# Optimization experiments

Measured on AMD Instinct MI355X. Metric: run time of the kernel, lower is better.

Reference implementation:

```python
import jax, jax.numpy as jnp
import numpy as np

N_NODES = 100000
N_EDGES = 200000
N_GRAPHS = 4096
NODE_DIM = 64
HID = 256
N_GAT = 4
NEG_SLOPE = 0.2
EPS = 1e-9


def setup_inputs() -> dict:
    key = jax.random.key(0)
    ks = jax.random.split(key, 16)
    node_feats = jax.random.normal(ks[0], (N_NODES, NODE_DIM), dtype=jnp.float32)
    src = jax.random.randint(ks[1], (N_EDGES,), 0, N_NODES)
    dst = jax.random.randint(ks[2], (N_EDGES,), 0, N_NODES)
    graph_ids = jnp.sort(jax.random.randint(ks[3], (N_NODES,), 0, N_GRAPHS))
    s = 1.0 / np.sqrt(HID)
    w_embed = jax.random.normal(ks[4], (NODE_DIM, HID), dtype=jnp.float32) / np.sqrt(NODE_DIM)
    b_embed = jnp.zeros((HID,), dtype=jnp.float32)
    gat_W = jax.random.normal(ks[5], (N_GAT, HID, HID), dtype=jnp.float32) * s
    gat_al = jax.random.normal(ks[6], (N_GAT, HID), dtype=jnp.float32) * s
    gat_ar = jax.random.normal(ks[7], (N_GAT, HID), dtype=jnp.float32) * s
    w1 = jax.random.normal(ks[8], (HID, HID // 2), dtype=jnp.float32) * s
    b1 = jnp.zeros((HID // 2,), dtype=jnp.float32)
    w2 = jax.random.normal(ks[9], (HID // 2, HID // 4), dtype=jnp.float32) / np.sqrt(HID // 2)
    b2 = jnp.zeros((HID // 4,), dtype=jnp.float32)
    w3 = jax.random.normal(ks[10], (HID // 4, 1), dtype=jnp.float32) / np.sqrt(HID // 4)
    b3 = jnp.zeros((1,), dtype=jnp.float32)
    return dict(node_feats=node_feats, src=src, dst=dst, graph_ids=graph_ids,
                w_embed=w_embed, b_embed=b_embed, gat_W=gat_W, gat_al=gat_al,
                gat_ar=gat_ar, w1=w1, b1=b1, w2=w2, b2=b2, w3=w3, b3=b3)


def _gat_layer(h, W, al, ar, src, dst):
    z = h @ W                                   # [N, HID]
    el = z @ al                                 # [N] source attention term
    er = z @ ar                                 # [N] destination attention term
    e = jax.nn.leaky_relu(el[src] + er[dst], NEG_SLOPE)   # [E]
    # segment softmax over edges grouped by destination node
    emax = jax.ops.segment_max(e, dst, num_segments=N_NODES)
    emax = jnp.where(jnp.isfinite(emax), emax, 0.0)
    ex = jnp.exp(e - emax[dst])
    esum = jax.ops.segment_sum(ex, dst, num_segments=N_NODES)
    alpha = ex / (esum[dst] + EPS)              # [E]
    m = jax.ops.segment_sum(alpha[:, None] * z[src], dst, num_segments=N_NODES)
    return jax.nn.relu(m + h)                   # residual + ReLU


def reference(node_feats, src, dst, graph_ids, w_embed, b_embed,
              gat_W, gat_al, gat_ar, w1, b1, w2, b2, w3, b3):
    h = node_feats @ w_embed + b_embed          # node embedding
    for l in range(N_GAT):
        h = _gat_layer(h, gat_W[l], gat_al[l], gat_ar[l], src, dst)
    g = jax.ops.segment_sum(h, graph_ids, num_segments=N_GRAPHS)  # sum pooling [G, HID]
    g = jax.nn.relu(g @ w1 + b1)
    g = jax.nn.relu(g @ w2 + b2)
    return g @ w3 + b3                          # [G, 1]
```

## Files before the change

### kernel.cpp

```cpp
#include <hip/hip_runtime.h>
#include <hip/hip_bf16.h>

#define N_NODES 100000
#define N_EDGES 200000
#define N_GRAPHS 4096
#define NODE_DIM 64
#define HID 256
#define N_GAT 4
#define NEG_SLOPE 0.2f
#define EPS 1e-9f
#define NB 98

typedef const __attribute__((address_space(1))) void gv_t;
typedef __attribute__((address_space(3))) void lv_t;
typedef __attribute__((ext_vector_type(8))) short bf16x8;
typedef __attribute__((ext_vector_type(4))) float f32x4;

__device__ __forceinline__ float b2f(unsigned short u) {
    return __uint_as_float(((unsigned)u) << 16);
}
__device__ __forceinline__ unsigned short f2b(float f) {
    unsigned u = __float_as_uint(f);
    return (unsigned short)((u + 0x7fffu + ((u >> 16) & 1u)) >> 16);
}

__global__ void convert_f32_bf16(const float* __restrict__ src,
                                 unsigned short* __restrict__ dst, int n4) {
    int i = blockIdx.x * 256 + threadIdx.x;
    if (i >= n4) return;
    float4 v = ((const float4*)src)[i];
    ushort4 o;
    o.x = f2b(v.x); o.y = f2b(v.y); o.z = f2b(v.z); o.w = f2b(v.w);
    ((ushort4*)dst)[i] = o;
}

__global__ __launch_bounds__(256) void transpose_bf16(const float* __restrict__ W,
                                                      unsigned short* __restrict__ Wt,
                                                      int K) {
    __shared__ float tile[32][33];
    const int kb = blockIdx.x * 32, cb = blockIdx.y * 32;
    const int tr = threadIdx.x >> 5, tc = threadIdx.x & 31;
#pragma unroll
    for (int i = 0; i < 4; ++i)
        tile[tr + i * 8][tc] = W[(size_t)(kb + tr + i * 8) * HID + cb + tc];
    __syncthreads();
#pragma unroll
    for (int i = 0; i < 4; ++i)
        Wt[(size_t)(cb + tr + i * 8) * K + kb + tc] = f2b(tile[tc][tr + i * 8]);
}

template <int K, bool BIAS, bool DOTS>
__global__ __launch_bounds__(256) void gemm_mfma(const unsigned short* __restrict__ Xb,
                                                 const unsigned short* __restrict__ Wt,
                                                 const float* __restrict__ bias,
                                                 unsigned short* __restrict__ Yb,
                                                 const float* __restrict__ al,
                                                 const float* __restrict__ ar,
                                                 float* __restrict__ el,
                                                 float* __restrict__ er,
                                                 int M) {
    constexpr int KC = 64;
    constexpr int NT = K / KC;
    __shared__ unsigned short xs[2][128 * KC];
    __shared__ unsigned short wsx[2][128 * KC];
    const int t = threadIdx.x, wv = t >> 6, ln = t & 63;
    const int wr2 = wv >> 1, wc2 = wv & 1;
    const long row0 = (long)blockIdx.x * 128;
    const int  col0 = blockIdx.y * 128;

    auto stage = [&](int buf, int k0) {
#pragma unroll
        for (int i = 0; i < 4; ++i) {
            const int chunk = wv * 4 + i;
            const int row = chunk * 8 + (ln >> 3);
            const int gsrc = (ln & 7) ^ (row & 7);
            long gr = row0 + row; if (gr >= M) gr = M - 1;
            const unsigned short* gp = Xb + gr * K + k0 + gsrc * 8;
            __builtin_amdgcn_global_load_lds((gv_t*)gp, (lv_t*)(&xs[buf][chunk * 512 + ln * 8]), 16, 0, 0);
        }
#pragma unroll
        for (int i = 0; i < 4; ++i) {
            const int chunk = wv * 4 + i;
            const int row = chunk * 8 + (ln >> 3);
            const int gsrc = (ln & 7) ^ (row & 7);
            const unsigned short* gp = Wt + (size_t)(col0 + row) * K + k0 + gsrc * 8;
            __builtin_amdgcn_global_load_lds((gv_t*)gp, (lv_t*)(&wsx[buf][chunk * 512 + ln * 8]), 16, 0, 0);
        }
    };

    f32x4 acc[4][4];
#pragma unroll
    for (int m = 0; m < 4; ++m)
#pragma unroll
        for (int n = 0; n < 4; ++n) acc[m][n] = (f32x4){0.f, 0.f, 0.f, 0.f};

    stage(0, 0);
    __syncthreads();

#pragma unroll
    for (int tt = 0; tt < NT; ++tt) {
        const int cur = tt & 1;
        if (tt + 1 < NT) stage(cur ^ 1, (tt + 1) * KC);

#pragma unroll
        for (int kk = 0; kk < 2; ++kk) {
            bf16x8 a[4], b[4];
            const int g = kk * 4 + (ln >> 4);
#pragma unroll
            for (int m = 0; m < 4; ++m) {
                const int row = wr2 * 64 + m * 16 + (ln & 15);
                const int s = g ^ (row & 7);
                a[m] = *(const bf16x8*)&xs[cur][row * 64 + s * 8];
            }
#pragma unroll
            for (int n = 0; n < 4; ++n) {
                const int row = wc2 * 64 + n * 16 + (ln & 15);
                const int s = g ^ (row & 7);
                b[n] = *(const bf16x8*)&wsx[cur][row * 64 + s * 8];
            }
#pragma unroll
            for (int m = 0; m < 4; ++m)
#pragma unroll
                for (int n = 0; n < 4; ++n)
                    acc[m][n] = __builtin_amdgcn_mfma_f32_16x16x32_bf16(a[m], b[n], acc[m][n], 0, 0, 0);
        }
        __syncthreads();
    }

    float bj[4];
#pragma unroll
    for (int n = 0; n < 4; ++n)
        bj[n] = BIAS ? bias[col0 + wc2 * 64 + n * 16 + (ln & 15)] : 0.f;

#pragma unroll
    for (int m = 0; m < 4; ++m) {
        const long rbase = row0 + wr2 * 64 + m * 16 + 4 * (ln >> 4);
#pragma unroll
        for (int n = 0; n < 4; ++n) {
            const int col = col0 + wc2 * 64 + n * 16 + (ln & 15);
#pragma unroll
            for (int q = 0; q < 4; ++q) {
                const long r = rbase + q;
                if (r >= M) continue;
                Yb[r * HID + col] = f2b(acc[m][n][q] + bj[n]);
            }
        }
    }

    if (DOTS) {
        float alv[4], arv[4];
#pragma unroll
        for (int n = 0; n < 4; ++n) {
            const int col = col0 + wc2 * 64 + n * 16 + (ln & 15);
            alv[n] = al[col];
            arv[n] = ar[col];
        }
#pragma unroll
        for (int m = 0; m < 4; ++m) {
#pragma unroll
            for (int q = 0; q < 4; ++q) {
                float pl = 0.f, pr = 0.f;
#pragma unroll
                for (int n = 0; n < 4; ++n) {
                    pl = fmaf(acc[m][n][q], alv[n], pl);
                    pr = fmaf(acc[m][n][q], arv[n], pr);
                }
#pragma unroll
                for (int o = 1; o < 16; o <<= 1) {
                    pl += __shfl_xor(pl, o);
                    pr += __shfl_xor(pr, o);
                }
                if ((ln & 15) == 0) {
                    const long r = row0 + wr2 * 64 + m * 16 + 4 * (ln >> 4) + q;
                    if (r < M) {
                        atomicAdd(&el[r], pl);
                        atomicAdd(&er[r], pr);
                    }
                }
            }
        }
    }
}

__global__ void hist_dst(const int* __restrict__ dst, int* __restrict__ deg) {
    int i = blockIdx.x * 256 + threadIdx.x;
    if (i < N_EDGES) atomicAdd(&deg[dst[i]], 1);
}

__global__ __launch_bounds__(1024) void scan_block(const int* __restrict__ deg,
                                                   int* __restrict__ sexc,
                                                   int* __restrict__ bsum) {
    int t = threadIdx.x, gid = blockIdx.x * 1024 + t;
    int v = (gid < N_NODES) ? deg[gid] : 0;
    int lane = t & 63, wv = t >> 6;
    int x = v;
#pragma unroll
    for (int o = 1; o < 64; o <<= 1) {
        int y = __shfl_up(x, o);
        if (lane >= o) x += y;
    }
    __shared__ int wsum[16];
    if (lane == 63) wsum[wv] = x;
    __syncthreads();
    if (t == 0) {
        int a = 0;
#pragma unroll
        for (int i = 0; i < 16; ++i) { int tt = wsum[i]; wsum[i] = a; a += tt; }
        bsum[blockIdx.x] = a;
    }
    __syncthreads();
    sexc[gid] = (x - v) + wsum[wv];
}

__global__ __launch_bounds__(128) void scan_partials(int* __restrict__ bsum,
                                                     int* __restrict__ offsets) {
    __shared__ int s[128];
    int t = threadIdx.x;
    int v = (t < NB) ? bsum[t] : 0;
    s[t] = v;
    __syncthreads();
    for (int o = 1; o < 128; o <<= 1) {
        int y = (t >= o) ? s[t - o] : 0;
        __syncthreads();
        s[t] += y;
        __syncthreads();
    }
    if (t < NB) bsum[t] = s[t] - v;
    if (t == 127) offsets[N_NODES] = s[127];
}

__global__ __launch_bounds__(1024) void scan_add(const int* __restrict__ sexc,
                                                 const int* __restrict__ bsum,
                                                 int* __restrict__ offsets,
                                                 int* __restrict__ cnt) {
    int gid = blockIdx.x * 1024 + threadIdx.x;
    if (gid < N_NODES) {
        int v = sexc[gid] + bsum[blockIdx.x];
        offsets[gid] = v;
        cnt[gid] = v;
    }
}

__global__ void csr_fill(const int* __restrict__ src, const int* __restrict__ dst,
                         int* __restrict__ cnt, int* __restrict__ csrc) {
    int i = blockIdx.x * 256 + threadIdx.x;
    if (i < N_EDGES) {
        int slot = atomicAdd(&cnt[dst[i]], 1);
        csrc[slot] = src[i];
    }
}

__global__ void graph_offsets(const int* __restrict__ gid, int* __restrict__ goff) {
    int g = blockIdx.x * 256 + threadIdx.x;
    if (g > N_GRAPHS) return;
    int lo = 0, hi = N_NODES;
    while (lo < hi) {
        int mid = (lo + hi) >> 1;
        if (gid[mid] < g) lo = mid + 1; else hi = mid;
    }
    goff[g] = lo;
}

__global__ __launch_bounds__(256) void alpha_kernel(const int* __restrict__ offs,
                                                    const int* __restrict__ csrc,
                                                    const float* __restrict__ el,
                                                    const float* __restrict__ er,
                                                    float* __restrict__ alpha) {
    int n = blockIdx.x * 256 + threadIdx.x;
    if (n >= N_NODES) return;
    const int beg = offs[n], end = offs[n + 1];
    if (beg == end) return;
    const float ern = er[n];
    float m = -3.4e38f;
    for (int c = beg; c < end; ++c) {
        float v = el[csrc[c]] + ern;
        v = (v >= 0.f) ? v : NEG_SLOPE * v;
        alpha[c] = v;
        m = fmaxf(m, v);
    }
    float s = 0.f;
    for (int c = beg; c < end; ++c) {
        float a = __expf(alpha[c] - m);
        alpha[c] = a;
        s += a;
    }
    const float inv = 1.f / (s + EPS);
    for (int c = beg; c < end; ++c) alpha[c] *= inv;
}

__global__ __launch_bounds__(256) void gather_attn(const int* __restrict__ offs,
                                                   const int* __restrict__ csrc,
                                                   const float* __restrict__ alpha,
                                                   const unsigned short* __restrict__ z,
                                                   unsigned short* __restrict__ Ab) {
    const int n = blockIdx.x * 4 + (threadIdx.x >> 6);
    const int lane = threadIdx.x & 63;
    const int beg = offs[n], end = offs[n + 1];

    float4 acc = make_float4(0.f, 0.f, 0.f, 0.f);
    int c = beg;
    for (; c + 1 < end; c += 2) {
        float a0 = alpha[c], a1 = alpha[c + 1];
        int s0 = csrc[c], s1 = csrc[c + 1];
        ushort4 z0 = ((const ushort4*)(z + (size_t)s0 * HID))[lane];
        ushort4 z1 = ((const ushort4*)(z + (size_t)s1 * HID))[lane];
        acc.x = fmaf(a0, b2f(z0.x), acc.x); acc.x = fmaf(a1, b2f(z1.x), acc.x);
        acc.y = fmaf(a0, b2f(z0.y), acc.y); acc.y = fmaf(a1, b2f(z1.y), acc.y);
        acc.z = fmaf(a0, b2f(z0.z), acc.z); acc.z = fmaf(a1, b2f(z1.z), acc.z);
        acc.w = fmaf(a0, b2f(z0.w), acc.w); acc.w = fmaf(a1, b2f(z1.w), acc.w);
    }
    if (c < end) {
        float a = alpha[c];
        int sc = csrc[c];
        ushort4 zz = ((const ushort4*)(z + (size_t)sc * HID))[lane];
        acc.x = fmaf(a, b2f(zz.x), acc.x);
        acc.y = fmaf(a, b2f(zz.y), acc.y);
        acc.z = fmaf(a, b2f(zz.z), acc.z);
        acc.w = fmaf(a, b2f(zz.w), acc.w);
    }

    ushort4* Ap = (ushort4*)(Ab + (size_t)n * HID);
    ushort4 hh = Ap[lane];
    ushort4 ob;
    ob.x = f2b(fmaxf(b2f(hh.x) + acc.x, 0.f));
    ob.y = f2b(fmaxf(b2f(hh.y) + acc.y, 0.f));
    ob.z = f2b(fmaxf(b2f(hh.z) + acc.z, 0.f));
    ob.w = f2b(fmaxf(b2f(hh.w) + acc.w, 0.f));
    Ap[lane] = ob;
}

__global__ __launch_bounds__(256) void pool_seg(const unsigned short* __restrict__ h,
                                                const int* __restrict__ goff,
                                                float* __restrict__ g) {
    const int gi = blockIdx.x, t = threadIdx.x;
    const int beg = goff[gi], end = goff[gi + 1];
    float acc = 0.f;
    for (int n = beg; n < end; ++n) acc += b2f(h[(size_t)n * HID + t]);
    g[(size_t)gi * HID + t] = acc;
}

__global__ void mlp_kernel(const float* __restrict__ g,
                           const float* __restrict__ w1, const float* __restrict__ b1,
                           const float* __restrict__ w2, const float* __restrict__ b2,
                           const float* __restrict__ w3, const float* __restrict__ b3,
                           float* __restrict__ out) {
    int gi = blockIdx.x, t = threadIdx.x;
    __shared__ float x[HID];
    __shared__ float y1[HID / 2];
    __shared__ float y2[HID / 4];
    x[t] = g[gi * HID + t];
    __syncthreads();
    if (t < HID / 2) {
        float a = b1[t];
#pragma unroll 8
        for (int k = 0; k < HID; ++k) a += x[k] * w1[k * (HID / 2) + t];
        y1[t] = fmaxf(a, 0.f);
    }
    __syncthreads();
    if (t < HID / 4) {
        float a = b2[t];
#pragma unroll 8
        for (int k = 0; k < HID / 2; ++k) a += y1[k] * w2[k * (HID / 4) + t];
        y2[t] = fmaxf(a, 0.f);
    }
    __syncthreads();
    if (t < 64) {
        float p = y2[t] * w3[t];
#pragma unroll
        for (int off = 32; off > 0; off >>= 1) p += __shfl_down(p, off);
        if (t == 0) out[gi] = p + b3[0];
    }
}

extern "C" void kernel_launch(void* const* d_in, const int* in_sizes, int n_in,
                              void* d_out, int out_size, void* d_ws, size_t ws_size,
                              hipStream_t stream) {
    const float* node_feats = (const float*)d_in[0];
    const int*   src        = (const int*)d_in[1];
    const int*   dst        = (const int*)d_in[2];
    const int*   graph_ids  = (const int*)d_in[3];
    const float* w_embed    = (const float*)d_in[4];
    const float* b_embed    = (const float*)d_in[5];
    const float* gat_W      = (const float*)d_in[6];
    const float* gat_al     = (const float*)d_in[7];
    const float* gat_ar     = (const float*)d_in[8];
    const float* w1         = (const float*)d_in[9];
    const float* b1         = (const float*)d_in[10];
    const float* w2         = (const float*)d_in[11];
    const float* b2         = (const float*)d_in[12];
    const float* w3         = (const float*)d_in[13];
    const float* b3         = (const float*)d_in[14];
    float* out = (float*)d_out;

    char* ws = (char*)d_ws;
    size_t off = 0;
    auto alloc = [&](size_t bytes) { char* p = ws + off; off += (bytes + 255) & ~size_t(255); return p; };
    unsigned short* Ab      = (unsigned short*)alloc((size_t)N_NODES * HID * 2);
    unsigned short* Zb      = (unsigned short*)alloc((size_t)N_NODES * HID * 2);
    unsigned short* Wt      = (unsigned short*)alloc((size_t)HID * HID * 2);
    float*          eler    = (float*)alloc((size_t)2 * N_NODES * 4);
    float*          alpha   = (float*)alloc((size_t)N_EDGES * 4);
    int*            deg     = (int*)alloc((size_t)N_NODES * 4);
    int*            cnt     = (int*)alloc((size_t)N_NODES * 4);
    int*            sexc    = (int*)alloc((size_t)NB * 1024 * 4);
    int*            bsum    = (int*)alloc(128 * 4);
    int*            offsets = (int*)alloc((size_t)(N_NODES + 1) * 4);
    int*            csrc    = (int*)alloc((size_t)N_EDGES * 4);
    int*            goff    = (int*)alloc((size_t)(N_GRAPHS + 1) * 4);
    float*          g       = (float*)alloc((size_t)N_GRAPHS * HID * 4);
    float*          el      = eler;
    float*          er      = eler + N_NODES;
    unsigned short* nfb     = Zb;

    hipMemsetAsync(deg, 0, (size_t)N_NODES * 4, stream);
    hist_dst<<<(N_EDGES + 255) / 256, 256, 0, stream>>>(dst, deg);
    scan_block<<<NB, 1024, 0, stream>>>(deg, sexc, bsum);
    scan_partials<<<1, 128, 0, stream>>>(bsum, offsets);
    scan_add<<<NB, 1024, 0, stream>>>(sexc, bsum, offsets, cnt);
    csr_fill<<<(N_EDGES + 255) / 256, 256, 0, stream>>>(src, dst, cnt, csrc);
    graph_offsets<<<(N_GRAPHS + 256) / 256, 256, 0, stream>>>(graph_ids, goff);

    dim3 ggrid((N_NODES + 127) / 128, HID / 128);

    convert_f32_bf16<<<(N_NODES * NODE_DIM / 4 + 255) / 256, 256, 0, stream>>>(node_feats, nfb, N_NODES * NODE_DIM / 4);
    transpose_bf16<<<dim3(NODE_DIM / 32, HID / 32), 256, 0, stream>>>(w_embed, Wt, NODE_DIM);
    gemm_mfma<NODE_DIM, true, false><<<ggrid, 256, 0, stream>>>(
        nfb, Wt, b_embed, Ab, nullptr, nullptr, nullptr, nullptr, N_NODES);

    for (int l = 0; l < N_GAT; ++l) {
        const float* W  = gat_W  + (size_t)l * HID * HID;
        const float* al = gat_al + (size_t)l * HID;
        const float* ar = gat_ar + (size_t)l * HID;

        transpose_bf16<<<dim3(HID / 32, HID / 32), 256, 0, stream>>>(W, Wt, HID);
        hipMemsetAsync(eler, 0, (size_t)2 * N_NODES * 4, stream);
        gemm_mfma<HID, false, true><<<ggrid, 256, 0, stream>>>(
            Ab, Wt, nullptr, Zb, al, ar, el, er, N_NODES);
        alpha_kernel<<<(N_NODES + 255) / 256, 256, 0, stream>>>(offsets, csrc, el, er, alpha);
        gather_attn<<<N_NODES / 4, 256, 0, stream>>>(offsets, csrc, alpha, Zb, Ab);
    }

    pool_seg<<<N_GRAPHS, 256, 0, stream>>>(Ab, goff, g);
    mlp_kernel<<<N_GRAPHS, HID, 0, stream>>>(g, w1, b1, w2, b2, w3, b3, out);
}
```

Measured before the change: 510.7 us.

## Fold attention vectors into weights and compute el/er in gather epilogue

Precomputes W·al and W·ar per layer so the attention scores can be taken directly from h, not from z. el/er move out of the GEMM: the first layer's come from a new dot kernel and later layers' from the gather kernel's epilogue. That removes the per-layer atomics, memset and weight transposes, since all weights are transposed once up front. The GEMM also gains an XCD-aware block swizzle and a coalesced store through swizzled LDS. Risk: el/er now come from bf16-rounded h rather than fp32 z, which shifts the rounding slightly.

```diff
diff --git a/kernel.cpp b/kernel.cpp
--- a/kernel.cpp
+++ b/kernel.cpp
@@ -34,9 +34,11 @@
     ((ushort4*)dst)[i] = o;
 }
 
-__global__ __launch_bounds__(256) void transpose_bf16(const float* __restrict__ W,
-                                                      unsigned short* __restrict__ Wt,
+__global__ __launch_bounds__(256) void transpose_bf16(const float* __restrict__ W0,
+                                                      unsigned short* __restrict__ Wt0,
                                                       int K) {
+    const float* W = W0 + (size_t)blockIdx.z * K * HID;
+    unsigned short* Wt = Wt0 + (size_t)blockIdx.z * K * HID;
     __shared__ float tile[32][33];
     const int kb = blockIdx.x * 32, cb = blockIdx.y * 32;
     const int tr = threadIdx.x >> 5, tc = threadIdx.x & 31;
@@ -49,15 +51,30 @@
         Wt[(size_t)(cb + tr + i * 8) * K + kb + tc] = f2b(tile[tc][tr + i * 8]);
 }
 
-template <int K, bool BIAS, bool DOTS>
+__global__ __launch_bounds__(256) void precompute_av(const unsigned short* __restrict__ Wt4,
+                                                     const float* __restrict__ gal,
+                                                     const float* __restrict__ gar,
+                                                     float* __restrict__ wal,
+                                                     float* __restrict__ war) {
+    const int l = blockIdx.x, k = threadIdx.x;
+    const unsigned short* Wt = Wt4 + (size_t)l * HID * HID;
+    const float* al = gal + l * HID;
+    const float* ar = gar + l * HID;
+    float a = 0.f, b = 0.f;
+    for (int c = 0; c < HID; ++c) {
+        float w = b2f(Wt[(size_t)c * HID + k]);
+        a = fmaf(w, al[c], a);
+        b = fmaf(w, ar[c], b);
+    }
+    wal[l * HID + k] = a;
+    war[l * HID + k] = b;
+}
+
+template <int K, bool BIAS>
 __global__ __launch_bounds__(256) void gemm_mfma(const unsigned short* __restrict__ Xb,
                                                  const unsigned short* __restrict__ Wt,
                                                  const float* __restrict__ bias,
                                                  unsigned short* __restrict__ Yb,
-                                                 const float* __restrict__ al,
-                                                 const float* __restrict__ ar,
-                                                 float* __restrict__ el,
-                                                 float* __restrict__ er,
                                                  int M) {
     constexpr int KC = 64;
     constexpr int NT = K / KC;
@@ -65,8 +82,13 @@
     __shared__ unsigned short wsx[2][128 * KC];
     const int t = threadIdx.x, wv = t >> 6, ln = t & 63;
     const int wr2 = wv >> 1, wc2 = wv & 1;
-    const long row0 = (long)blockIdx.x * 128;
-    const int  col0 = blockIdx.y * 128;
+
+    const int nwg = gridDim.x;
+    const int q8 = nwg >> 3, r8 = nwg & 7;
+    const int xcd = blockIdx.x & 7, idx = blockIdx.x >> 3;
+    const int sw = (xcd < r8) ? xcd * (q8 + 1) + idx : r8 * (q8 + 1) + (xcd - r8) * q8 + idx;
+    const long row0 = (long)(sw >> 1) * 128;
+    const int  col0 = (sw & 1) * 128;
 
     auto stage = [&](int buf, int k0) {
 #pragma unroll
@@ -132,53 +154,28 @@
     for (int n = 0; n < 4; ++n)
         bj[n] = BIAS ? bias[col0 + wc2 * 64 + n * 16 + (ln & 15)] : 0.f;
 
+    char* ep = (char*)&xs[0][0];
 #pragma unroll
     for (int m = 0; m < 4; ++m) {
-        const long rbase = row0 + wr2 * 64 + m * 16 + 4 * (ln >> 4);
+        const int rb = wr2 * 64 + m * 16 + 4 * (ln >> 4);
 #pragma unroll
         for (int n = 0; n < 4; ++n) {
-            const int col = col0 + wc2 * 64 + n * 16 + (ln & 15);
-#pragma unroll
-            for (int q = 0; q < 4; ++q) {
-                const long r = rbase + q;
-                if (r >= M) continue;
-                Yb[r * HID + col] = f2b(acc[m][n][q] + bj[n]);
+            const int colB = (wc2 * 64 + n * 16 + (ln & 15)) * 2;
+#pragma unroll
+            for (int qq = 0; qq < 4; ++qq) {
+                const int rr = rb + qq;
+                *(unsigned short*)(ep + rr * 256 + (colB ^ ((rr & 7) << 4))) = f2b(acc[m][n][qq] + bj[n]);
             }
         }
     }
-
-    if (DOTS) {
-        float alv[4], arv[4];
-#pragma unroll
-        for (int n = 0; n < 4; ++n) {
-            const int col = col0 + wc2 * 64 + n * 16 + (ln & 15);
-            alv[n] = al[col];
-            arv[n] = ar[col];
-        }
-#pragma unroll
-        for (int m = 0; m < 4; ++m) {
-#pragma unroll
-            for (int q = 0; q < 4; ++q) {
-                float pl = 0.f, pr = 0.f;
-#pragma unroll
-                for (int n = 0; n < 4; ++n) {
-                    pl = fmaf(acc[m][n][q], alv[n], pl);
-                    pr = fmaf(acc[m][n][q], arv[n], pr);
-                }
-#pragma unroll
-                for (int o = 1; o < 16; o <<= 1) {
-                    pl += __shfl_xor(pl, o);
-                    pr += __shfl_xor(pr, o);
-                }
-                if ((ln & 15) == 0) {
-                    const long r = row0 + wr2 * 64 + m * 16 + 4 * (ln >> 4) + q;
-                    if (r < M) {
-                        atomicAdd(&el[r], pl);
-                        atomicAdd(&er[r], pr);
-                    }
-                }
-            }
-        }
+    __syncthreads();
+#pragma unroll
+    for (int j = 0; j < 8; ++j) {
+        const int row = t >> 1;
+        const int cb = (t & 1) * 128 + j * 16;
+        uint4 v = *(const uint4*)(ep + row * 256 + (cb ^ ((row & 7) << 4)));
+        const long r = row0 + row;
+        if (r < M) *(uint4*)(Yb + r * HID + col0 + (cb >> 1)) = v;
     }
 }
 
@@ -259,6 +256,25 @@
         if (gid[mid] < g) lo = mid + 1; else hi = mid;
     }
     goff[g] = lo;
+}
+
+__global__ void node_dots_b(const unsigned short* __restrict__ h,
+                            const float* __restrict__ wal,
+                            const float* __restrict__ war,
+                            float* __restrict__ el, float* __restrict__ er) {
+    int n = blockIdx.x * 4 + (threadIdx.x >> 6);
+    int lane = threadIdx.x & 63;
+    ushort4 zz = ((const ushort4*)(h + (size_t)n * HID))[lane];
+    float4 a = ((const float4*)wal)[lane];
+    float4 b = ((const float4*)war)[lane];
+    float pl = b2f(zz.x) * a.x + b2f(zz.y) * a.y + b2f(zz.z) * a.z + b2f(zz.w) * a.w;
+    float pr = b2f(zz.x) * b.x + b2f(zz.y) * b.y + b2f(zz.z) * b.z + b2f(zz.w) * b.w;
+#pragma unroll
+    for (int off = 32; off > 0; off >>= 1) {
+        pl += __shfl_down(pl, off);
+        pr += __shfl_down(pr, off);
+    }
+    if (lane == 0) { el[n] = pl; er[n] = pr; }
 }
 
 __global__ __launch_bounds__(256) void alpha_kernel(const int* __restrict__ offs,
@@ -292,7 +308,11 @@
                                                    const int* __restrict__ csrc,
                                                    const float* __restrict__ alpha,
                                                    const unsigned short* __restrict__ z,
-                                                   unsigned short* __restrict__ Ab) {
+                                                   unsigned short* __restrict__ Ab,
+                                                   const float* __restrict__ waln,
+                                                   const float* __restrict__ warn,
+                                                   float* __restrict__ el,
+                                                   float* __restrict__ er) {
     const int n = blockIdx.x * 4 + (threadIdx.x >> 6);
     const int lane = threadIdx.x & 63;
     const int beg = offs[n], end = offs[n + 1];
@@ -321,12 +341,26 @@
 
     ushort4* Ap = (ushort4*)(Ab + (size_t)n * HID);
     ushort4 hh = Ap[lane];
+    float h0 = fmaxf(b2f(hh.x) + acc.x, 0.f);
+    float h1 = fmaxf(b2f(hh.y) + acc.y, 0.f);
+    float h2 = fmaxf(b2f(hh.z) + acc.z, 0.f);
+    float h3 = fmaxf(b2f(hh.w) + acc.w, 0.f);
     ushort4 ob;
-    ob.x = f2b(fmaxf(b2f(hh.x) + acc.x, 0.f));
-    ob.y = f2b(fmaxf(b2f(hh.y) + acc.y, 0.f));
-    ob.z = f2b(fmaxf(b2f(hh.z) + acc.z, 0.f));
-    ob.w = f2b(fmaxf(b2f(hh.w) + acc.w, 0.f));
+    ob.x = f2b(h0); ob.y = f2b(h1); ob.z = f2b(h2); ob.w = f2b(h3);
     Ap[lane] = ob;
+
+    if (waln) {
+        float4 wa = ((const float4*)waln)[lane];
+        float4 wb = ((const float4*)warn)[lane];
+        float pl = h0 * wa.x + h1 * wa.y + h2 * wa.z + h3 * wa.w;
+        float pr = h0 * wb.x + h1 * wb.y + h2 * wb.z + h3 * wb.w;
+#pragma unroll
+        for (int o = 32; o > 0; o >>= 1) {
+            pl += __shfl_down(pl, o);
+            pr += __shfl_down(pr, o);
+        }
+        if (lane == 0) { el[n] = pl; er[n] = pr; }
+    }
 }
 
 __global__ __launch_bounds__(256) void pool_seg(const unsigned short* __restrict__ h,
@@ -397,7 +431,10 @@
     auto alloc = [&](size_t bytes) { char* p = ws + off; off += (bytes + 255) & ~size_t(255); return p; };
     unsigned short* Ab      = (unsigned short*)alloc((size_t)N_NODES * HID * 2);
     unsigned short* Zb      = (unsigned short*)alloc((size_t)N_NODES * HID * 2);
-    unsigned short* Wt      = (unsigned short*)alloc((size_t)HID * HID * 2);
+    unsigned short* Wte     = (unsigned short*)alloc((size_t)HID * NODE_DIM * 2);
+    unsigned short* Wtg     = (unsigned short*)alloc((size_t)N_GAT * HID * HID * 2);
+    float*          wal     = (float*)alloc((size_t)N_GAT * HID * 4);
+    float*          war     = (float*)alloc((size_t)N_GAT * HID * 4);
     float*          eler    = (float*)alloc((size_t)2 * N_NODES * 4);
     float*          alpha   = (float*)alloc((size_t)N_EDGES * 4);
     int*            deg     = (int*)alloc((size_t)N_NODES * 4);
@@ -420,24 +457,25 @@
     csr_fill<<<(N_EDGES + 255) / 256, 256, 0, stream>>>(src, dst, cnt, csrc);
     graph_offsets<<<(N_GRAPHS + 256) / 256, 256, 0, stream>>>(graph_ids, goff);
 
-    dim3 ggrid((N_NODES + 127) / 128, HID / 128);
-
+    transpose_bf16<<<dim3(NODE_DIM / 32, HID / 32, 1), 256, 0, stream>>>(w_embed, Wte, NODE_DIM);
+    transpose_bf16<<<dim3(HID / 32, HID / 32, N_GAT), 256, 0, stream>>>(gat_W, Wtg, HID);
+    precompute_av<<<N_GAT, 256, 0, stream>>>(Wtg, gat_al, gat_ar, wal, war);
     convert_f32_bf16<<<(N_NODES * NODE_DIM / 4 + 255) / 256, 256, 0, stream>>>(node_feats, nfb, N_NODES * NODE_DIM / 4);
-    transpose_bf16<<<dim3(NODE_DIM / 32, HID / 32), 256, 0, stream>>>(w_embed, Wt, NODE_DIM);
-    gemm_mfma<NODE_DIM, true, false><<<ggrid, 256, 0, stream>>>(
-        nfb, Wt, b_embed, Ab, nullptr, nullptr, nullptr, nullptr, N_NODES);
+
+    const int ntm = (N_NODES + 127) / 128;
+    const int ngrid = ntm * 2;
+
+    gemm_mfma<NODE_DIM, true><<<ngrid, 256, 0, stream>>>(nfb, Wte, b_embed, Ab, N_NODES);
+    node_dots_b<<<N_NODES / 4, 256, 0, stream>>>(Ab, wal, war, el, er);
 
     for (int l = 0; l < N_GAT; ++l) {
-        const float* W  = gat_W  + (size_t)l * HID * HID;
-        const float* al = gat_al + (size_t)l * HID;
-        const float* ar = gat_ar + (size_t)l * HID;
-
-        transpose_bf16<<<dim3(HID / 32, HID / 32), 256, 0, stream>>>(W, Wt, HID);
-        hipMemsetAsync(eler, 0, (size_t)2 * N_NODES * 4, stream);
-        gemm_mfma<HID, false, true><<<ggrid, 256, 0, stream>>>(
-            Ab, Wt, nullptr, Zb, al, ar, el, er, N_NODES);
+        gemm_mfma<HID, false><<<ngrid, 256, 0, stream>>>(
+            Ab, Wtg + (size_t)l * HID * HID, nullptr, Zb, N_NODES);
         alpha_kernel<<<(N_NODES + 255) / 256, 256, 0, stream>>>(offsets, csrc, el, er, alpha);
-        gather_attn<<<N_NODES / 4, 256, 0, stream>>>(offsets, csrc, alpha, Zb, Ab);
+        const float* waln = (l < N_GAT - 1) ? wal + (l + 1) * HID : nullptr;
+        const float* warn = (l < N_GAT - 1) ? war + (l + 1) * HID : nullptr;
+        gather_attn<<<N_NODES / 4, 256, 0, stream>>>(offsets, csrc, alpha, Zb, Ab,
+                                                     waln, warn, el, er);
     }
 
     pool_seg<<<N_GRAPHS, 256, 0, stream>>>(Ab, goff, g);
```

New measurement: 509.1 us. No clear change (-0.3%).
